# Optimization experiments

Hardware: AMD Instinct MI355X
Metric: run time of the kernel (lower is better)

Reference implementation:

```python
import jax, jax.numpy as jnp
import numpy as np

IN_FEATURES = 4096
OUT_FEATURES = 4096
BATCH = 4096
MASK_DENSITY = 0.05  # typical power-grid neighborhood sparsity


def setup_inputs() -> dict:
    key = jax.random.key(0)
    k_x, k_w, k_b, k_m = jax.random.split(key, 4)
    x = jax.random.normal(k_x, (BATCH, IN_FEATURES), dtype=jnp.float32)
    # kaiming_uniform_(a=sqrt(5)) -> uniform(-bound, bound), bound = sqrt(6/((1+5)*fan_in)) = 1/sqrt(fan_in)
    w_bound = 1.0 / np.sqrt(IN_FEATURES)
    weight = jax.random.uniform(k_w, (OUT_FEATURES, IN_FEATURES), dtype=jnp.float32,
                                minval=-w_bound, maxval=w_bound)
    bias = jax.random.uniform(k_b, (OUT_FEATURES,), dtype=jnp.float32,
                              minval=-w_bound, maxval=w_bound)
    # fixed binary neighborhood filter (non-trainable), int-valued {0,1} as in the torch module
    myFilter = (jax.random.uniform(k_m, (OUT_FEATURES, IN_FEATURES)) < MASK_DENSITY).astype(jnp.float32)
    return {"x": x, "weight": weight, "bias": bias, "myFilter": myFilter}


def reference(x, weight, bias, myFilter):
    # F.linear(input, weight * myFilter, bias): y = x @ (W * M)^T + b
    masked_w = weight * myFilter                      # [out, in]
    return jnp.einsum('bi,oi->bo', x, masked_w) + bias  # [batch, out]
```

## Files before the change

### kernel.cpp

```cpp
#include <hip/hip_runtime.h>
#include <hip/hip_bf16.h>
#include <stdint.h>

#define IN_F   4096
#define OUT_F  4096
#define BATCH  4096

typedef __bf16 bf16x8_t __attribute__((ext_vector_type(8)));
typedef float  f32x4_t  __attribute__((ext_vector_type(4)));
typedef float  f32x4v   __attribute__((ext_vector_type(4)));
typedef unsigned short u16x4v __attribute__((ext_vector_type(4)));

#define AS_GLOBAL(p) ((const __attribute__((address_space(1))) void*)(p))
#define AS_LDS(p)    ((__attribute__((address_space(3))) void*)(p))

__device__ __forceinline__ unsigned short f32_to_bf16_rne(float f) {
    union { float f; uint32_t u; } v; v.f = f;
    uint32_t u = v.u;
    u += 0x7FFFu + ((u >> 16) & 1u);
    return (unsigned short)(u >> 16);
}

__global__ __launch_bounds__(256)
void convert_kernel(const float* __restrict__ x,
                    const float* __restrict__ w,
                    const float* __restrict__ m,
                    unsigned short* __restrict__ xb,
                    unsigned short* __restrict__ wb) {
    const int64_t i0 = (int64_t)blockIdx.x * 512 + threadIdx.x;
#pragma unroll
    for (int u = 0; u < 2; ++u) {
        const int64_t i = i0 + u * 256;
        f32x4v xv = __builtin_nontemporal_load(&((const f32x4v*)x)[i]);
        f32x4v wv = __builtin_nontemporal_load(&((const f32x4v*)w)[i]);
        f32x4v mv = __builtin_nontemporal_load(&((const f32x4v*)m)[i]);
        u16x4v xo, wo;
        xo.x = f32_to_bf16_rne(xv.x);
        xo.y = f32_to_bf16_rne(xv.y);
        xo.z = f32_to_bf16_rne(xv.z);
        xo.w = f32_to_bf16_rne(xv.w);
        wo.x = f32_to_bf16_rne(wv.x * mv.x);
        wo.y = f32_to_bf16_rne(wv.y * mv.y);
        wo.z = f32_to_bf16_rne(wv.z * mv.z);
        wo.w = f32_to_bf16_rne(wv.w * mv.w);
        ((u16x4v*)xb)[i] = xo;
        ((u16x4v*)wb)[i] = wo;
    }
}

#define BM 256
#define BN 256
#define BK 64
#define NT (IN_F / BK)

__global__ __launch_bounds__(512, 2)
void gemm_8phase_kernel(const unsigned short* __restrict__ A,
                        const unsigned short* __restrict__ B,
                        const float* __restrict__ bias,
                        float* __restrict__ C) {
    __shared__ __align__(16) unsigned short sA[2][2][128 * 64];
    __shared__ __align__(16) unsigned short sB[2][2][128 * 64];

    const int t    = threadIdx.x;
    const int wv   = t >> 6;
    const int lane = t & 63;
    const int quad = lane >> 4;
    const int l16  = lane & 15;
    const int wr   = wv >> 2;
    const int wc   = wv & 3;
    const int bhalf = wc >> 1;
    const int brow0 = (wc & 1) * 64;

    const int bid = blockIdx.x;
    const int swz = (bid & 7) * 32 + (bid >> 3);
    const int bm  = (swz >> 4) * BM;
    const int bn  = (swz & 15) * BN;

    const int srow = t >> 3;
    const int scol = 8 * ((t & 7) ^ (srow & 7));
    const unsigned short* gA = A + (int64_t)(bm + srow) * IN_F + scol;
    const unsigned short* gB = B + (int64_t)(bn + srow) * IN_F + scol;
    const int ldsoff = t * 16;

#define STAGE_A(TT, h)                                                        \
    do {                                                                      \
        _Pragma("unroll")                                                     \
        for (int rr = 0; rr < 2; ++rr)                                        \
            __builtin_amdgcn_global_load_lds(                                 \
                AS_GLOBAL(gA + (int64_t)((h) * 128 + rr * 64) * IN_F + (TT) * BK), \
                AS_LDS((char*)sA[(TT) & 1][h] + rr * 8192 + ldsoff), 16, 0, 0); \
    } while (0)
#define STAGE_B(TT, h)                                                        \
    do {                                                                      \
        _Pragma("unroll")                                                     \
        for (int rr = 0; rr < 2; ++rr)                                        \
            __builtin_amdgcn_global_load_lds(                                 \
                AS_GLOBAL(gB + (int64_t)((h) * 128 + rr * 64) * IN_F + (TT) * BK), \
                AS_LDS((char*)sB[(TT) & 1][h] + rr * 8192 + ldsoff), 16, 0, 0); \
    } while (0)

    f32x4_t acc[8][4];
#pragma unroll
    for (int mi = 0; mi < 8; ++mi)
#pragma unroll
        for (int ni = 0; ni < 4; ++ni)
            acc[mi][ni] = (f32x4_t){0.f, 0.f, 0.f, 0.f};

    STAGE_A(0, 0); STAGE_A(0, 1); STAGE_B(0, 0); STAGE_B(0, 1);
    STAGE_B(1, 0); STAGE_B(1, 1); STAGE_A(1, 0);
    asm volatile("s_waitcnt vmcnt(6)" ::: "memory");
    __builtin_amdgcn_s_barrier();

    for (int T = 0; T < NT; ++T) {
        const unsigned short* myA = sA[T & 1][wr];
        const unsigned short* myB = sB[T & 1][bhalf];

        bf16x8_t af[4][2], bf0[2][2], bf1[2][2];

#pragma unroll
        for (int j = 0; j < 4; ++j) {
            const int row = j * 16 + l16;
#pragma unroll
            for (int ks = 0; ks < 2; ++ks)
                af[j][ks] = *(const bf16x8_t*)(myA + row * 64 +
                                ((ks * 4 + quad) ^ (row & 7)) * 8);
        }
#pragma unroll
        for (int j = 0; j < 2; ++j) {
            const int row = brow0 + j * 16 + l16;
#pragma unroll
            for (int ks = 0; ks < 2; ++ks)
                bf0[j][ks] = *(const bf16x8_t*)(myB + row * 64 +
                                ((ks * 4 + quad) ^ (row & 7)) * 8);
        }
        if (T + 1 < NT) STAGE_A(T + 1, 1);
        __builtin_amdgcn_s_barrier();
        asm volatile("s_waitcnt lgkmcnt(0)" ::: "memory");
        __builtin_amdgcn_s_setprio(1);
#pragma unroll
        for (int mi = 0; mi < 4; ++mi)
#pragma unroll
            for (int ni = 0; ni < 2; ++ni)
#pragma unroll
                for (int ks = 0; ks < 2; ++ks)
                    acc[mi][ni] = __builtin_amdgcn_mfma_f32_16x16x32_bf16(
                        af[mi][ks], bf0[ni][ks], acc[mi][ni], 0, 0, 0);
        __builtin_amdgcn_s_setprio(0);
        __builtin_amdgcn_s_barrier();

#pragma unroll
        for (int j = 0; j < 2; ++j) {
            const int row = brow0 + (j + 2) * 16 + l16;
#pragma unroll
            for (int ks = 0; ks < 2; ++ks)
                bf1[j][ks] = *(const bf16x8_t*)(myB + row * 64 +
                                ((ks * 4 + quad) ^ (row & 7)) * 8);
        }
        __builtin_amdgcn_s_barrier();
        asm volatile("s_waitcnt lgkmcnt(0)" ::: "memory");
        __builtin_amdgcn_s_setprio(1);
#pragma unroll
        for (int mi = 0; mi < 4; ++mi)
#pragma unroll
            for (int ni = 0; ni < 2; ++ni)
#pragma unroll
                for (int ks = 0; ks < 2; ++ks)
                    acc[mi][ni + 2] = __builtin_amdgcn_mfma_f32_16x16x32_bf16(
                        af[mi][ks], bf1[ni][ks], acc[mi][ni + 2], 0, 0, 0);
        __builtin_amdgcn_s_setprio(0);
        __builtin_amdgcn_s_barrier();

#pragma unroll
        for (int j = 0; j < 4; ++j) {
            const int row = (j + 4) * 16 + l16;
#pragma unroll
            for (int ks = 0; ks < 2; ++ks)
                af[j][ks] = *(const bf16x8_t*)(myA + row * 64 +
                                ((ks * 4 + quad) ^ (row & 7)) * 8);
        }
        if (T + 2 < NT) STAGE_B(T + 2, 0);
        __builtin_amdgcn_s_barrier();
        asm volatile("s_waitcnt lgkmcnt(0)" ::: "memory");
        __builtin_amdgcn_s_setprio(1);
#pragma unroll
        for (int mi = 0; mi < 4; ++mi)
#pragma unroll
            for (int ni = 0; ni < 2; ++ni)
#pragma unroll
                for (int ks = 0; ks < 2; ++ks)
                    acc[mi + 4][ni + 2] = __builtin_amdgcn_mfma_f32_16x16x32_bf16(
                        af[mi][ks], bf1[ni][ks], acc[mi + 4][ni + 2], 0, 0, 0);
        __builtin_amdgcn_s_setprio(0);
        __builtin_amdgcn_s_barrier();

        if (T + 2 < NT) { STAGE_B(T + 2, 1); STAGE_A(T + 2, 0); }
        __builtin_amdgcn_s_barrier();
        __builtin_amdgcn_s_setprio(1);
#pragma unroll
        for (int mi = 0; mi < 4; ++mi)
#pragma unroll
            for (int ni = 0; ni < 2; ++ni)
#pragma unroll
                for (int ks = 0; ks < 2; ++ks)
                    acc[mi + 4][ni] = __builtin_amdgcn_mfma_f32_16x16x32_bf16(
                        af[mi][ks], bf0[ni][ks], acc[mi + 4][ni], 0, 0, 0);
        __builtin_amdgcn_s_setprio(0);
        if (T < NT - 2)
            asm volatile("s_waitcnt vmcnt(6)" ::: "memory");
        else if (T < NT - 1)
            asm volatile("s_waitcnt vmcnt(0)" ::: "memory");
        __builtin_amdgcn_s_barrier();
    }

    float bv[4];
#pragma unroll
    for (int ni = 0; ni < 4; ++ni)
        bv[ni] = bias[bn + wc * 64 + ni * 16 + l16];

#pragma unroll
    for (int mi = 0; mi < 8; ++mi) {
        const int row0 = bm + wr * 128 + mi * 16 + quad * 4;
#pragma unroll
        for (int ni = 0; ni < 4; ++ni) {
            const int col = bn + wc * 64 + ni * 16 + l16;
#pragma unroll
            for (int reg = 0; reg < 4; ++reg)
                C[(int64_t)(row0 + reg) * OUT_F + col] = acc[mi][ni][reg] + bv[ni];
        }
    }
#undef STAGE_A
#undef STAGE_B
}

__global__ void fallback_gemm_kernel(const float* __restrict__ x,
                                     const float* __restrict__ w,
                                     const float* __restrict__ bias,
                                     const float* __restrict__ m,
                                     float* __restrict__ y) {
    __shared__ float sx[16][17];
    __shared__ float sw[16][17];
    const int tx = threadIdx.x, ty = threadIdx.y;
    const int row = blockIdx.y * 16 + ty;
    const int col = blockIdx.x * 16 + tx;
    float acc = 0.f;
    for (int k0 = 0; k0 < IN_F; k0 += 16) {
        sx[ty][tx] = x[(int64_t)row * IN_F + k0 + tx];
        const int64_t widx = (int64_t)(blockIdx.x * 16 + ty) * IN_F + k0 + tx;
        sw[ty][tx] = w[widx] * m[widx];
        __syncthreads();
#pragma unroll
        for (int kk = 0; kk < 16; ++kk)
            acc += sx[ty][kk] * sw[tx][kk];
        __syncthreads();
    }
    y[(int64_t)row * OUT_F + col] = acc + bias[col];
}

extern "C" void kernel_launch(void* const* d_in, const int* in_sizes, int n_in,
                              void* d_out, int out_size, void* d_ws, size_t ws_size,
                              hipStream_t stream) {
    const float* x    = (const float*)d_in[0];
    const float* w    = (const float*)d_in[1];
    const float* bias = (const float*)d_in[2];
    const float* m    = (const float*)d_in[3];
    float* y = (float*)d_out;

    const size_t need = (size_t)2 * (size_t)OUT_F * (size_t)IN_F * sizeof(unsigned short);

    if (ws_size >= need) {
        unsigned short* xb = (unsigned short*)d_ws;
        unsigned short* wb = xb + (size_t)BATCH * IN_F;

        convert_kernel<<<8192, 256, 0, stream>>>(x, w, m, xb, wb);

        gemm_8phase_kernel<<<256, 512, 0, stream>>>(xb, wb, bias, y);
    } else {
        dim3 grid(OUT_F / 16, BATCH / 16);
        dim3 block(16, 16);
        fallback_gemm_kernel<<<grid, block, 0, stream>>>(x, w, bias, m, y);
    }
}
```

Before: 326.7 us.

## Collapse 8-phase GEMM mainloop into two-barrier schedule

The per-K-tile loop goes from eight barrier-separated phases to two larger MFMA blocks, with a pair of barriers at the end of each iteration around the global-to-LDS staging for tile T+2. All B fragments are loaded up front, and sched_barrier fences stop the compiler from moving code across the sync points. The aim is to cut barrier and lgkm wait overhead and let the compiler interleave LDS reads with MFMAs. In exchange, staging loads no longer overlap with compute phases the way they did, register pressure rises from holding b0 and b1 together, and the hand-tuned ping-pong between the two waves sharing a SIMD is lost.

```diff
diff --git a/kernel.cpp b/kernel.cpp
--- a/kernel.cpp
+++ b/kernel.cpp
@@ -54,10 +54,10 @@
 #define NT (IN_F / BK)
 
 __global__ __launch_bounds__(512, 2)
-void gemm_8phase_kernel(const unsigned short* __restrict__ A,
-                        const unsigned short* __restrict__ B,
-                        const float* __restrict__ bias,
-                        float* __restrict__ C) {
+void gemm_2bar_kernel(const unsigned short* __restrict__ A,
+                      const unsigned short* __restrict__ B,
+                      const float* __restrict__ bias,
+                      float* __restrict__ C) {
     __shared__ __align__(16) unsigned short sA[2][2][128 * 64];
     __shared__ __align__(16) unsigned short sB[2][2][128 * 64];
 
@@ -110,12 +110,13 @@
     STAGE_B(1, 0); STAGE_B(1, 1); STAGE_A(1, 0);
     asm volatile("s_waitcnt vmcnt(6)" ::: "memory");
     __builtin_amdgcn_s_barrier();
+    __builtin_amdgcn_sched_barrier(0);
 
     for (int T = 0; T < NT; ++T) {
         const unsigned short* myA = sA[T & 1][wr];
         const unsigned short* myB = sB[T & 1][bhalf];
 
-        bf16x8_t af[4][2], bf0[2][2], bf1[2][2];
+        bf16x8_t af[4][2], b0[2][2], b1[2][2];
 
 #pragma unroll
         for (int j = 0; j < 4; ++j) {
@@ -130,34 +131,19 @@
             const int row = brow0 + j * 16 + l16;
 #pragma unroll
             for (int ks = 0; ks < 2; ++ks)
-                bf0[j][ks] = *(const bf16x8_t*)(myB + row * 64 +
-                                ((ks * 4 + quad) ^ (row & 7)) * 8);
-        }
-        if (T + 1 < NT) STAGE_A(T + 1, 1);
-        __builtin_amdgcn_s_barrier();
-        asm volatile("s_waitcnt lgkmcnt(0)" ::: "memory");
-        __builtin_amdgcn_s_setprio(1);
-#pragma unroll
-        for (int mi = 0; mi < 4; ++mi)
-#pragma unroll
-            for (int ni = 0; ni < 2; ++ni)
-#pragma unroll
-                for (int ks = 0; ks < 2; ++ks)
-                    acc[mi][ni] = __builtin_amdgcn_mfma_f32_16x16x32_bf16(
-                        af[mi][ks], bf0[ni][ks], acc[mi][ni], 0, 0, 0);
-        __builtin_amdgcn_s_setprio(0);
-        __builtin_amdgcn_s_barrier();
-
+                b0[j][ks] = *(const bf16x8_t*)(myB + row * 64 +
+                                ((ks * 4 + quad) ^ (row & 7)) * 8);
+        }
 #pragma unroll
         for (int j = 0; j < 2; ++j) {
             const int row = brow0 + (j + 2) * 16 + l16;
 #pragma unroll
             for (int ks = 0; ks < 2; ++ks)
-                bf1[j][ks] = *(const bf16x8_t*)(myB + row * 64 +
-                                ((ks * 4 + quad) ^ (row & 7)) * 8);
-        }
-        __builtin_amdgcn_s_barrier();
-        asm volatile("s_waitcnt lgkmcnt(0)" ::: "memory");
+                b1[j][ks] = *(const bf16x8_t*)(myB + row * 64 +
+                                ((ks * 4 + quad) ^ (row & 7)) * 8);
+        }
+        if (T + 1 < NT) STAGE_A(T + 1, 1);
+
         __builtin_amdgcn_s_setprio(1);
 #pragma unroll
         for (int mi = 0; mi < 4; ++mi)
@@ -165,10 +151,17 @@
             for (int ni = 0; ni < 2; ++ni)
 #pragma unroll
                 for (int ks = 0; ks < 2; ++ks)
+                    acc[mi][ni] = __builtin_amdgcn_mfma_f32_16x16x32_bf16(
+                        af[mi][ks], b0[ni][ks], acc[mi][ni], 0, 0, 0);
+#pragma unroll
+        for (int mi = 0; mi < 4; ++mi)
+#pragma unroll
+            for (int ni = 0; ni < 2; ++ni)
+#pragma unroll
+                for (int ks = 0; ks < 2; ++ks)
                     acc[mi][ni + 2] = __builtin_amdgcn_mfma_f32_16x16x32_bf16(
-                        af[mi][ks], bf1[ni][ks], acc[mi][ni + 2], 0, 0, 0);
+                        af[mi][ks], b1[ni][ks], acc[mi][ni + 2], 0, 0, 0);
         __builtin_amdgcn_s_setprio(0);
-        __builtin_amdgcn_s_barrier();
 
 #pragma unroll
         for (int j = 0; j < 4; ++j) {
@@ -178,9 +171,7 @@
                 af[j][ks] = *(const bf16x8_t*)(myA + row * 64 +
                                 ((ks * 4 + quad) ^ (row & 7)) * 8);
         }
-        if (T + 2 < NT) STAGE_B(T + 2, 0);
-        __builtin_amdgcn_s_barrier();
-        asm volatile("s_waitcnt lgkmcnt(0)" ::: "memory");
+
         __builtin_amdgcn_s_setprio(1);
 #pragma unroll
         for (int mi = 0; mi < 4; ++mi)
@@ -189,27 +180,28 @@
 #pragma unroll
                 for (int ks = 0; ks < 2; ++ks)
                     acc[mi + 4][ni + 2] = __builtin_amdgcn_mfma_f32_16x16x32_bf16(
-                        af[mi][ks], bf1[ni][ks], acc[mi + 4][ni + 2], 0, 0, 0);
+                        af[mi][ks], b1[ni][ks], acc[mi + 4][ni + 2], 0, 0, 0);
+#pragma unroll
+        for (int mi = 0; mi < 4; ++mi)
+#pragma unroll
+            for (int ni = 0; ni < 2; ++ni)
+#pragma unroll
+                for (int ks = 0; ks < 2; ++ks)
+                    acc[mi + 4][ni] = __builtin_amdgcn_mfma_f32_16x16x32_bf16(
+                        af[mi][ks], b0[ni][ks], acc[mi + 4][ni], 0, 0, 0);
         __builtin_amdgcn_s_setprio(0);
-        __builtin_amdgcn_s_barrier();
-
-        if (T + 2 < NT) { STAGE_B(T + 2, 1); STAGE_A(T + 2, 0); }
-        __builtin_amdgcn_s_barrier();
-        __builtin_amdgcn_s_setprio(1);
-#pragma unroll
-        for (int mi = 0; mi < 4; ++mi)
-#pragma unroll
-            for (int ni = 0; ni < 2; ++ni)
-#pragma unroll
-                for (int ks = 0; ks < 2; ++ks)
-                    acc[mi + 4][ni] = __builtin_amdgcn_mfma_f32_16x16x32_bf16(
-                        af[mi][ks], bf0[ni][ks], acc[mi + 4][ni], 0, 0, 0);
-        __builtin_amdgcn_s_setprio(0);
-        if (T < NT - 2)
-            asm volatile("s_waitcnt vmcnt(6)" ::: "memory");
-        else if (T < NT - 1)
-            asm volatile("s_waitcnt vmcnt(0)" ::: "memory");
-        __builtin_amdgcn_s_barrier();
+
+        if (T + 1 < NT) {
+            __builtin_amdgcn_s_barrier();
+            __builtin_amdgcn_sched_barrier(0);
+            if (T + 2 < NT) { STAGE_B(T + 2, 0); STAGE_B(T + 2, 1); STAGE_A(T + 2, 0); }
+            if (T < NT - 2)
+                asm volatile("s_waitcnt vmcnt(6)" ::: "memory");
+            else
+                asm volatile("s_waitcnt vmcnt(0)" ::: "memory");
+            __builtin_amdgcn_s_barrier();
+            __builtin_amdgcn_sched_barrier(0);
+        }
     }
 
     float bv[4];
@@ -273,7 +265,7 @@
 
         convert_kernel<<<8192, 256, 0, stream>>>(x, w, m, xb, wb);
 
-        gemm_8phase_kernel<<<256, 512, 0, stream>>>(xb, wb, bias, y);
+        gemm_2bar_kernel<<<256, 512, 0, stream>>>(xb, wb, bias, y);
     } else {
         dim3 grid(OUT_F / 16, BATCH / 16);
         dim3 block(16, 16);
```

Result: faster. 310.2 us (-5.0%).
